# Performance work log

Measured on AMD Instinct MI355X. Metric: run time of the kernel, lower is better.

The kernel has to match this reference:

```python
import jax, jax.numpy as jnp
import numpy as np

CONTEXT_DIM = 64
HIDDEN = 512
BS = 1024
SEQ = 168
TWIN = 96


def setup_inputs() -> dict:
    key = jax.random.key(0)
    k0, k1, k2, k3 = jax.random.split(key, 4)
    x_dyn = jax.random.normal(k0, (BS, SEQ, CONTEXT_DIM), jnp.float32)
    y_flow = jax.random.normal(k1, (BS, SEQ, 1), jnp.float32)
    input_dim = CONTEXT_DIM + 1 + 1
    W = jax.random.normal(k2, (input_dim + HIDDEN, HIDDEN * 4), jnp.float32) * 0.02
    b = jnp.zeros((HIDDEN * 4,), jnp.float32)
    Wo = jax.random.normal(k3, (HIDDEN, 1), jnp.float32) * 0.02
    bo = jnp.zeros((1,), jnp.float32)
    return {"x_dyn": x_dyn, "y_flow": y_flow, "W": W, "b": b,
            "Wo": Wo, "bo": bo, "twin_idx": TWIN}


def _cell(inp, h, c, W, b, hidden):
    # fused gate GEMM: [bs, input_dim+hidden] @ [input_dim+hidden, 4*hidden]
    gates = jnp.concatenate([inp, h], axis=1) @ W + b
    i, f, g, o = jnp.split(gates, 4, axis=1)
    i = jax.nn.sigmoid(i)
    f = jax.nn.sigmoid(f)
    o = jax.nn.sigmoid(o)
    g = jnp.tanh(g)
    c_next = f * c + i * g
    h_next = o * jnp.tanh(c_next)
    return h_next, c_next


def reference(x_dyn, y_flow, W, b, Wo, bo, twin_idx):
    bs, seq_len, _ = x_dyn.shape
    hidden = W.shape[1] // 4
    h0 = jnp.zeros((bs, hidden), x_dyn.dtype)
    c0 = jnp.zeros((bs, hidden), x_dyn.dtype)
    zeros_col = jnp.zeros((bs, 1), x_dyn.dtype)
    ones_col = jnp.ones((bs, 1), x_dyn.dtype)

    # Phase 1: teacher-forced steps t in [0, twin_idx), h_since_tw = 0
    def step1(carry, xs):
        h, c = carry
        x_t, y_t = xs
        inp = jnp.concatenate([x_t, y_t, zeros_col], axis=1)
        h, c = _cell(inp, h, c, W, b, hidden)
        pred = h @ Wo + bo  # [bs, 1]
        return (h, c), pred

    xs1 = (jnp.swapaxes(x_dyn[:, :twin_idx], 0, 1),
           jnp.swapaxes(y_flow[:, :twin_idx], 0, 1))
    (h, c), preds1 = jax.lax.scan(step1, (h0, c0), xs1)  # preds1: [twin_idx, bs, 1]
    last_out = preds1[-1]

    n2 = seq_len - 1 - twin_idx
    h_vals = (jnp.arange(n2, dtype=x_dyn.dtype) + 1.0) / 24.0

    def step2(carry, xs):
        h, c, last = carry
        x_t, hv = xs
        inp = jnp.concatenate([x_t, last, hv * ones_col], axis=1)
        h, c = _cell(inp, h, c, W, b, hidden)
        last = h @ Wo + bo
        return (h, c, last), last

    xs2 = (jnp.swapaxes(x_dyn[:, twin_idx:seq_len - 1], 0, 1), h_vals)
    _, preds2 = jax.lax.scan(step2, (h, c, last_out), xs2)  # [n2, bs, 1]

    preds = jnp.concatenate([preds1, preds2], axis=0)  # [seq_len-1, bs, 1]
    return jnp.swapaxes(preds, 0, 1)  # [bs, seq_len-1, 1]
```

## Files before the change

### kernel.cpp

```cpp
#include <hip/hip_runtime.h>


#define HIDDEN 512
#define SEQ    168
#define NSTEP  167
#define BS     1024
#define CTX    64
#define KM     576
#define KP     584
#define MTILE  128
#define SGRID  512
#define PGRID  256
#define NTHR   256
#define WTELEM (2 * 32 * KP)

typedef __attribute__((ext_vector_type(8))) short s16x8;
typedef __attribute__((ext_vector_type(4))) float f32x4;

static __device__ __forceinline__ unsigned short bf16_rne(float f) {
    union { float f; unsigned int u; } v; v.f = f;
    unsigned int r = v.u + 0x7FFFu + ((v.u >> 16) & 1u);
    return (unsigned short)(r >> 16);
}
static __device__ __forceinline__ float bf16_to_f(unsigned short h) {
    union { float f; unsigned int u; } v; v.u = ((unsigned int)h) << 16;
    return v.f;
}
static __device__ __forceinline__ float sigmoid_(float x) {
    x = fminf(fmaxf(x, -80.f), 80.f);
    return 1.0f / (1.0f + __expf(-x));
}
static __device__ __forceinline__ float tanh_(float x) {
    float ax = fminf(fabsf(x), 40.f);
    float e = __expf(-2.0f * ax);
    float r = (1.0f - e) / (1.0f + e);
    return copysignf(r, x);
}

__global__ void lstm_prep(const float* __restrict__ x_dyn, float* __restrict__ out,
                          const float* __restrict__ bo_p,
                          unsigned short* __restrict__ aHi, unsigned short* __restrict__ aLo,
                          float* __restrict__ cst)
{
    const int gthr = blockIdx.x * NTHR + threadIdx.x;
    const int gstr = PGRID * NTHR;
    const float bo = *bo_p;
    for (int i = gthr; i < BS * NSTEP; i += gstr) out[i] = bo;
    for (int i = gthr; i < BS * HIDDEN; i += gstr) cst[i] = 0.f;
    for (int i = gthr; i < BS * 256; i += gstr) {
        const int b = i >> 8, j = i & 255;
        ((unsigned int*)aHi)[b * 288 + 32 + j] = 0u;
        ((unsigned int*)aLo)[b * 288 + 32 + j] = 0u;
    }
    for (int i = gthr; i < BS * CTX; i += gstr) {
        const int b = i >> 6, col = i & 63;
        const float v = x_dyn[(size_t)b * SEQ * CTX + col];
        const unsigned short hi = bf16_rne(v);
        aHi[(size_t)b * KM + col] = hi;
        aLo[(size_t)b * KM + col] = bf16_rne(v - bf16_to_f(hi));
    }
}

__global__ void wprep(const float* __restrict__ Wg, unsigned short* __restrict__ wpl)
{
    const int gthr = blockIdx.x * NTHR + threadIdx.x;
    const int gstr = PGRID * NTHR;
    for (int i = gthr; i < 64 * 32 * KP; i += gstr) {
        const int kp = i % KP;
        const int c  = (i / KP) & 31;
        const int nt = i / (KP * 32);
        unsigned short hi = 0, lo = 0;
        if (kp < KM) {
            const int wrow = (kp < 64) ? kp : (kp + 2);
            const int wcol = (2 * (c >> 4) + ((c >> 3) & 1)) * 512 + nt * 8 + (c & 7);
            const float v = Wg[(size_t)wrow * 2048 + wcol];
            hi = bf16_rne(v);
            lo = bf16_rne(v - bf16_to_f(hi));
        }
        const size_t base = (size_t)nt * WTELEM + (size_t)c * KP + kp;
        wpl[base] = hi;
        wpl[base + 32 * KP] = lo;
    }
}

__global__ __launch_bounds__(NTHR, 2)
void lstm_step(const float* __restrict__ x_dyn, const float* __restrict__ y_flow,
               const float* __restrict__ Wg, const float* __restrict__ bias,
               const float* __restrict__ Wo, const int* __restrict__ twin_p,
               float* __restrict__ out, unsigned short* __restrict__ aHi,
               unsigned short* __restrict__ aLo, float* __restrict__ cst,
               const unsigned short* __restrict__ wpl, int t)
{
    extern __shared__ unsigned char smem_raw[];
    unsigned short* whi = (unsigned short*)smem_raw;
    unsigned short* wlo = whi + 32 * KP;
    float* a64s = (float*)(wlo + 32 * KP);

    const int tid = threadIdx.x, bid = blockIdx.x;
    const int nt = bid >> 3;
    const int m0 = (bid & 7) * MTILE;
    const int lane = tid & 63, wv = tid >> 6;
    const int ln15 = lane & 15, kg = lane >> 4;
    const int twin = *twin_p;

    const int par = t & 1, pn = par ^ 1;
    const unsigned short* aH = aHi + (size_t)par * BS * KM;
    const unsigned short* aL = aLo + (size_t)par * BS * KM;
    unsigned short* nH = aHi + (size_t)pn * BS * KM;
    unsigned short* nL = aLo + (size_t)pn * BS * KM;
    const float hv = (t < twin) ? 0.f : (float)(t - twin + 1) * (1.f / 24.f);

    const unsigned short* wsrc = wpl + (size_t)nt * WTELEM;
#if __has_builtin(__builtin_amdgcn_global_load_lds)
    for (int c = wv; c < 73; c += 4) {
        __builtin_amdgcn_global_load_lds(
            (const __attribute__((address_space(1))) void*)(wsrc + c * 512 + lane * 8),
            (__attribute__((address_space(3))) void*)(smem_raw + c * 1024),
            16, 0, 0);
    }
#else
    for (int idx = tid; idx < WTELEM / 8; idx += NTHR) {
        *(s16x8*)((unsigned short*)smem_raw + idx * 8) = *(const s16x8*)(wsrc + idx * 8);
    }
#endif

    if (tid < MTILE) {
        const int b = m0 + tid;
        float v;
        if (t < twin) v = y_flow[(size_t)b * SEQ + t];
        else if (t > 0) v = out[(size_t)b * NSTEP + (t - 1)];
        else v = 0.f;
        a64s[tid] = v;
    }
    __syncthreads();

    if (tid < 128) {
        const int b = m0 + nt * 2 + (tid >> 6), col = tid & 63;
        const float v = x_dyn[((size_t)b * SEQ + (t + 1)) * CTX + col];
        const unsigned short hi = bf16_rne(v);
        nH[(size_t)b * KM + col] = hi;
        nL[(size_t)b * KM + col] = bf16_rne(v - bf16_to_f(hi));
    }

    float w64c[2], basec[2];
    #pragma unroll
    for (int ns = 0; ns < 2; ++ns) {
        const int wcol = (2 * ns + (ln15 >> 3)) * 512 + nt * 8 + (ln15 & 7);
        w64c[ns]  = Wg[(size_t)64 * 2048 + wcol];
        basec[ns] = fmaf(hv, Wg[(size_t)65 * 2048 + wcol], bias[wcol]);
    }
    const int u = nt * 8 + (ln15 & 7);
    const float wo_u = Wo[u];
    const bool lo_half = (ln15 < 8);

    const size_t aoff0 = (size_t)(m0 + wv * 32 + ln15) * KM + kg * 8;
    const size_t aoff1 = aoff0 + (size_t)16 * KM;

    f32x4 acc[2][2];
    #pragma unroll
    for (int ms = 0; ms < 2; ++ms)
        #pragma unroll
        for (int ns = 0; ns < 2; ++ns) acc[ms][ns] = (f32x4){0.f, 0.f, 0.f, 0.f};

    #pragma unroll
    for (int half = 0; half < 2; ++half) {
        s16x8 Ah[9][2], Al[9][2];
        #pragma unroll
        for (int j = 0; j < 9; ++j) {
            const size_t k0 = (size_t)(half * 9 + j) * 32;
            Ah[j][0] = *(const s16x8*)(aH + aoff0 + k0);
            Ah[j][1] = *(const s16x8*)(aH + aoff1 + k0);
            Al[j][0] = *(const s16x8*)(aL + aoff0 + k0);
            Al[j][1] = *(const s16x8*)(aL + aoff1 + k0);
        }
        #pragma unroll
        for (int j = 0; j < 9; ++j) {
            const int k0 = (half * 9 + j) * 32;
            s16x8 bh[2], bl[2];
            #pragma unroll
            for (int ns = 0; ns < 2; ++ns) {
                const int boff = (ns * 16 + ln15) * KP + k0 + kg * 8;
                bh[ns] = *(const s16x8*)(whi + boff);
                bl[ns] = *(const s16x8*)(wlo + boff);
            }
            #pragma unroll
            for (int ns = 0; ns < 2; ++ns)
                #pragma unroll
                for (int ms = 0; ms < 2; ++ms) {
                    acc[ms][ns] = __builtin_amdgcn_mfma_f32_16x16x32_bf16(Ah[j][ms], bh[ns], acc[ms][ns], 0, 0, 0);
                    acc[ms][ns] = __builtin_amdgcn_mfma_f32_16x16x32_bf16(Ah[j][ms], bl[ns], acc[ms][ns], 0, 0, 0);
                    acc[ms][ns] = __builtin_amdgcn_mfma_f32_16x16x32_bf16(Al[j][ms], bh[ns], acc[ms][ns], 0, 0, 0);
                }
        }
    }

    #pragma unroll
    for (int ms = 0; ms < 2; ++ms) {
        #pragma unroll
        for (int r = 0; r < 4; ++r) {
            const int rl = wv * 32 + ms * 16 + kg * 4 + r;
            const int b = m0 + rl;
            const float a64v = a64s[rl];
            const float pre0 = acc[ms][0][r] + fmaf(a64v, w64c[0], basec[0]);
            const float pre1 = acc[ms][1][r] + fmaf(a64v, w64c[1], basec[1]);
            const float q0 = __shfl_xor(pre0, 8, 16);
            const float q1 = __shfl_xor(pre1, 8, 16);
            const float pi = lo_half ? pre0 : q0;
            const float pf = lo_half ? q0 : pre0;
            const float pg = lo_half ? pre1 : q1;
            const float po = lo_half ? q1 : pre1;
            const float i_ = sigmoid_(pi);
            const float f_ = sigmoid_(pf);
            const float g_ = tanh_(pg);
            const float o_ = sigmoid_(po);
            const size_t ci = (size_t)b * HIDDEN + u;
            const float c = f_ * cst[ci] + i_ * g_;
            const float h = o_ * tanh_(c);
            if (lo_half) {
                cst[ci] = c;
                const unsigned short hh = bf16_rne(h);
                nH[(size_t)b * KM + 64 + u] = hh;
                nL[(size_t)b * KM + 64 + u] = bf16_rne(h - bf16_to_f(hh));
            }
            float p = lo_half ? h * wo_u : 0.f;
            p += __shfl_xor(p, 1, 16);
            p += __shfl_xor(p, 2, 16);
            p += __shfl_xor(p, 4, 16);
            p += __shfl_xor(p, 8, 16);
            if (ln15 == 0) atomicAdd(&out[(size_t)b * NSTEP + t], p);
        }
    }
}

extern "C" void kernel_launch(void* const* d_in, const int* in_sizes, int n_in,
                              void* d_out, int out_size, void* d_ws, size_t ws_size,
                              hipStream_t stream) {
    (void)in_sizes; (void)n_in; (void)out_size; (void)ws_size;
    const float* x_dyn  = (const float*)d_in[0];
    const float* y_flow = (const float*)d_in[1];
    const float* Wg     = (const float*)d_in[2];
    const float* bias   = (const float*)d_in[3];
    const float* Wo     = (const float*)d_in[4];
    const float* bo     = (const float*)d_in[5];
    const int*   twin   = (const int*)d_in[6];
    float* out = (float*)d_out;

    unsigned short* aHi = (unsigned short*)d_ws;
    unsigned short* aLo = aHi + (size_t)2 * BS * KM;
    float* cst = (float*)(aLo + (size_t)2 * BS * KM);
    unsigned short* wpl = (unsigned short*)(cst + (size_t)BS * HIDDEN);

    const unsigned int smem = (2u * 32u * KP) * 2u + MTILE * 4u;

    (void)hipFuncSetAttribute((const void*)lstm_step,
                              hipFuncAttributeMaxDynamicSharedMemorySize, (int)smem);

    lstm_prep<<<dim3(PGRID), dim3(NTHR), 0, stream>>>(x_dyn, out, bo, aHi, aLo, cst);
    wprep<<<dim3(PGRID), dim3(NTHR), 0, stream>>>(Wg, wpl);

    for (int t = 0; t < NSTEP; ++t) {
        lstm_step<<<dim3(SGRID), dim3(NTHR), smem, stream>>>(
            x_dyn, y_flow, Wg, bias, Wo, twin, out, aHi, aLo, cst, wpl, t);
    }
}
```

Measured before the change: 5.099 ms.

## Replace per-step kernel launches with persistent cooperative kernel using grid sync

Runs all 167 recurrent steps inside one cooperative kernel with grid.sync between steps, and stages each block's weight slice into LDS only once instead of once per step. This removes per-step launch overhead and the repeated weight reload. It also switches the A-operand loads to inline-asm global loads followed by an explicit vmcnt wait, and reads the previous prediction with an atomic load. It depends on 512 blocks being co-resident at two blocks per CU, and falls back to the per-step launch loop if the cooperative launch fails.

```diff
diff --git a/kernel.cpp b/kernel.cpp
--- a/kernel.cpp
+++ b/kernel.cpp
@@ -1,4 +1,7 @@
 #include <hip/hip_runtime.h>
+#include <hip/hip_cooperative_groups.h>
+
+namespace cg = cooperative_groups;
 
 
 #define HIDDEN 512
@@ -35,6 +38,11 @@
     float e = __expf(-2.0f * ax);
     float r = (1.0f - e) / (1.0f + e);
     return copysignf(r, x);
+}
+static __device__ __forceinline__ s16x8 gload16(const unsigned short* p) {
+    s16x8 r;
+    asm volatile("global_load_dwordx4 %0, %1, off" : "=v"(r) : "v"(p));
+    return r;
 }
 
 __global__ void lstm_prep(const float* __restrict__ x_dyn, float* __restrict__ out,
@@ -83,26 +91,28 @@
     }
 }
 
-__global__ __launch_bounds__(NTHR, 2)
-void lstm_step(const float* __restrict__ x_dyn, const float* __restrict__ y_flow,
-               const float* __restrict__ Wg, const float* __restrict__ bias,
-               const float* __restrict__ Wo, const int* __restrict__ twin_p,
-               float* __restrict__ out, unsigned short* __restrict__ aHi,
-               unsigned short* __restrict__ aLo, float* __restrict__ cst,
-               const unsigned short* __restrict__ wpl, int t)
-{
-    extern __shared__ unsigned char smem_raw[];
-    unsigned short* whi = (unsigned short*)smem_raw;
-    unsigned short* wlo = whi + 32 * KP;
-    float* a64s = (float*)(wlo + 32 * KP);
-
-    const int tid = threadIdx.x, bid = blockIdx.x;
-    const int nt = bid >> 3;
-    const int m0 = (bid & 7) * MTILE;
-    const int lane = tid & 63, wv = tid >> 6;
-    const int ln15 = lane & 15, kg = lane >> 4;
-    const int twin = *twin_p;
-
+static __device__ __forceinline__ void stage_w(const unsigned short* __restrict__ wpl,
+                                               unsigned char* smem_raw, int nt, int wv, int lane)
+{
+    const unsigned short* wsrc = wpl + (size_t)nt * WTELEM;
+    for (int c = wv; c < 73; c += 4) {
+        __builtin_amdgcn_global_load_lds(
+            (const __attribute__((address_space(1))) void*)(wsrc + c * 512 + lane * 8),
+            (__attribute__((address_space(3))) void*)(smem_raw + c * 1024),
+            16, 0, 0);
+    }
+}
+
+static __device__ __forceinline__ void step_core(
+    int t, int twin, int tid, int nt, int m0,
+    const float* __restrict__ x_dyn, const float* __restrict__ y_flow,
+    float* __restrict__ out, float* __restrict__ cst,
+    unsigned short* __restrict__ aHi, unsigned short* __restrict__ aLo,
+    const unsigned short* whi, const unsigned short* wlo, float* a64s,
+    const float* w64c, const float* w65c, const float* biasc,
+    float wo_u, int u, int wv, int ln15, int kg, bool lo_half,
+    size_t aoff0, size_t aoff1)
+{
     const int par = t & 1, pn = par ^ 1;
     const unsigned short* aH = aHi + (size_t)par * BS * KM;
     const unsigned short* aL = aLo + (size_t)par * BS * KM;
@@ -110,25 +120,12 @@
     unsigned short* nL = aLo + (size_t)pn * BS * KM;
     const float hv = (t < twin) ? 0.f : (float)(t - twin + 1) * (1.f / 24.f);
 
-    const unsigned short* wsrc = wpl + (size_t)nt * WTELEM;
-#if __has_builtin(__builtin_amdgcn_global_load_lds)
-    for (int c = wv; c < 73; c += 4) {
-        __builtin_amdgcn_global_load_lds(
-            (const __attribute__((address_space(1))) void*)(wsrc + c * 512 + lane * 8),
-            (__attribute__((address_space(3))) void*)(smem_raw + c * 1024),
-            16, 0, 0);
-    }
-#else
-    for (int idx = tid; idx < WTELEM / 8; idx += NTHR) {
-        *(s16x8*)((unsigned short*)smem_raw + idx * 8) = *(const s16x8*)(wsrc + idx * 8);
-    }
-#endif
-
     if (tid < MTILE) {
         const int b = m0 + tid;
         float v;
         if (t < twin) v = y_flow[(size_t)b * SEQ + t];
-        else if (t > 0) v = out[(size_t)b * NSTEP + (t - 1)];
+        else if (t > 0) v = __hip_atomic_load(&out[(size_t)b * NSTEP + (t - 1)],
+                                              __ATOMIC_RELAXED, __HIP_MEMORY_SCOPE_AGENT);
         else v = 0.f;
         a64s[tid] = v;
     }
@@ -142,19 +139,9 @@
         nL[(size_t)b * KM + col] = bf16_rne(v - bf16_to_f(hi));
     }
 
-    float w64c[2], basec[2];
-    #pragma unroll
-    for (int ns = 0; ns < 2; ++ns) {
-        const int wcol = (2 * ns + (ln15 >> 3)) * 512 + nt * 8 + (ln15 & 7);
-        w64c[ns]  = Wg[(size_t)64 * 2048 + wcol];
-        basec[ns] = fmaf(hv, Wg[(size_t)65 * 2048 + wcol], bias[wcol]);
-    }
-    const int u = nt * 8 + (ln15 & 7);
-    const float wo_u = Wo[u];
-    const bool lo_half = (ln15 < 8);
-
-    const size_t aoff0 = (size_t)(m0 + wv * 32 + ln15) * KM + kg * 8;
-    const size_t aoff1 = aoff0 + (size_t)16 * KM;
+    float basec2[2];
+    basec2[0] = fmaf(hv, w65c[0], biasc[0]);
+    basec2[1] = fmaf(hv, w65c[1], biasc[1]);
 
     f32x4 acc[2][2];
     #pragma unroll
@@ -168,11 +155,13 @@
         #pragma unroll
         for (int j = 0; j < 9; ++j) {
             const size_t k0 = (size_t)(half * 9 + j) * 32;
-            Ah[j][0] = *(const s16x8*)(aH + aoff0 + k0);
-            Ah[j][1] = *(const s16x8*)(aH + aoff1 + k0);
-            Al[j][0] = *(const s16x8*)(aL + aoff0 + k0);
-            Al[j][1] = *(const s16x8*)(aL + aoff1 + k0);
-        }
+            Ah[j][0] = gload16(aH + aoff0 + k0);
+            Ah[j][1] = gload16(aH + aoff1 + k0);
+            Al[j][0] = gload16(aL + aoff0 + k0);
+            Al[j][1] = gload16(aL + aoff1 + k0);
+        }
+        asm volatile("s_waitcnt vmcnt(0)" ::: "memory");
+        __builtin_amdgcn_sched_barrier(0);
         #pragma unroll
         for (int j = 0; j < 9; ++j) {
             const int k0 = (half * 9 + j) * 32;
@@ -201,8 +190,8 @@
             const int rl = wv * 32 + ms * 16 + kg * 4 + r;
             const int b = m0 + rl;
             const float a64v = a64s[rl];
-            const float pre0 = acc[ms][0][r] + fmaf(a64v, w64c[0], basec[0]);
-            const float pre1 = acc[ms][1][r] + fmaf(a64v, w64c[1], basec[1]);
+            const float pre0 = acc[ms][0][r] + fmaf(a64v, w64c[0], basec2[0]);
+            const float pre1 = acc[ms][1][r] + fmaf(a64v, w64c[1], basec2[1]);
             const float q0 = __shfl_xor(pre0, 8, 16);
             const float q1 = __shfl_xor(pre1, 8, 16);
             const float pi = lo_half ? pre0 : q0;
@@ -232,6 +221,74 @@
     }
 }
 
+#define LANE_SETUP                                                              \
+    const int tid = threadIdx.x, bid = blockIdx.x;                              \
+    const int nt = bid >> 3;                   \
+    const int m0 = (bid & 7) * MTILE;              \
+    const int lane = tid & 63, wv = tid >> 6, ln15 = lane & 15, kg = lane >> 4; \
+    const int twin = *twin_p;                                                   \
+    float w64c[2], w65c[2], biasc[2];                                           \
+    _Pragma("unroll")                                                           \
+    for (int ns = 0; ns < 2; ++ns) {                                            \
+        const int wcol = (2 * ns + (ln15 >> 3)) * 512 + nt * 8 + (ln15 & 7);    \
+        w64c[ns]  = Wg[(size_t)64 * 2048 + wcol];                               \
+        w65c[ns]  = Wg[(size_t)65 * 2048 + wcol];                               \
+        biasc[ns] = bias[wcol];                                                 \
+    }                                                                           \
+    const int u = nt * 8 + (ln15 & 7);                                          \
+    const float wo_u = Wo[u];                                                   \
+    const bool lo_half = (ln15 < 8);                                            \
+    const size_t aoff0 = (size_t)(m0 + wv * 32 + ln15) * KM + kg * 8;           \
+    const size_t aoff1 = aoff0 + (size_t)16 * KM;
+
+__global__ __launch_bounds__(NTHR, 2)
+void lstm_persist(const float* __restrict__ x_dyn, const float* __restrict__ y_flow,
+                  const float* __restrict__ Wg, const float* __restrict__ bias,
+                  const float* __restrict__ Wo, const int* __restrict__ twin_p,
+                  float* __restrict__ out, unsigned short* __restrict__ aHi,
+                  unsigned short* __restrict__ aLo, float* __restrict__ cst,
+                  const unsigned short* __restrict__ wpl)
+{
+    cg::grid_group grid = cg::this_grid();
+    extern __shared__ unsigned char smem_raw[];
+    unsigned short* whi = (unsigned short*)smem_raw;
+    unsigned short* wlo = whi + 32 * KP;
+    float* a64s = (float*)(wlo + 32 * KP);
+
+    LANE_SETUP
+
+    stage_w(wpl, smem_raw, nt, wv, lane);
+
+    for (int t = 0; t < NSTEP; ++t) {
+        step_core(t, twin, tid, nt, m0, x_dyn, y_flow, out, cst, aHi, aLo,
+                  whi, wlo, a64s, w64c, w65c, biasc, wo_u, u, wv, ln15, kg,
+                  lo_half, aoff0, aoff1);
+        if (t != NSTEP - 1) grid.sync();
+    }
+}
+
+__global__ __launch_bounds__(NTHR, 2)
+void lstm_step(const float* __restrict__ x_dyn, const float* __restrict__ y_flow,
+               const float* __restrict__ Wg, const float* __restrict__ bias,
+               const float* __restrict__ Wo, const int* __restrict__ twin_p,
+               float* __restrict__ out, unsigned short* __restrict__ aHi,
+               unsigned short* __restrict__ aLo, float* __restrict__ cst,
+               const unsigned short* __restrict__ wpl, int t)
+{
+    extern __shared__ unsigned char smem_raw[];
+    unsigned short* whi = (unsigned short*)smem_raw;
+    unsigned short* wlo = whi + 32 * KP;
+    float* a64s = (float*)(wlo + 32 * KP);
+
+    LANE_SETUP
+
+    stage_w(wpl, smem_raw, nt, wv, lane);
+
+    step_core(t, twin, tid, nt, m0, x_dyn, y_flow, out, cst, aHi, aLo,
+              whi, wlo, a64s, w64c, w65c, biasc, wo_u, u, wv, ln15, kg,
+              lo_half, aoff0, aoff1);
+}
+
 extern "C" void kernel_launch(void* const* d_in, const int* in_sizes, int n_in,
                               void* d_out, int out_size, void* d_ws, size_t ws_size,
                               hipStream_t stream) {
@@ -252,14 +309,24 @@
 
     const unsigned int smem = (2u * 32u * KP) * 2u + MTILE * 4u;
 
+    (void)hipFuncSetAttribute((const void*)lstm_persist,
+                              hipFuncAttributeMaxDynamicSharedMemorySize, (int)smem);
     (void)hipFuncSetAttribute((const void*)lstm_step,
                               hipFuncAttributeMaxDynamicSharedMemorySize, (int)smem);
 
     lstm_prep<<<dim3(PGRID), dim3(NTHR), 0, stream>>>(x_dyn, out, bo, aHi, aLo, cst);
     wprep<<<dim3(PGRID), dim3(NTHR), 0, stream>>>(Wg, wpl);
 
-    for (int t = 0; t < NSTEP; ++t) {
-        lstm_step<<<dim3(SGRID), dim3(NTHR), smem, stream>>>(
-            x_dyn, y_flow, Wg, bias, Wo, twin, out, aHi, aLo, cst, wpl, t);
-    }
-}
+    void* kargs[] = {(void*)&x_dyn, (void*)&y_flow, (void*)&Wg, (void*)&bias,
+                     (void*)&Wo, (void*)&twin, (void*)&out,
+                     (void*)&aHi, (void*)&aLo, (void*)&cst, (void*)&wpl};
+    hipError_t rc = hipLaunchCooperativeKernel((const void*)lstm_persist,
+                                               dim3(SGRID), dim3(NTHR), kargs,
+                                               smem, stream);
+    if (rc != hipSuccess) {
+        for (int t = 0; t < NSTEP; ++t) {
+            lstm_step<<<dim3(SGRID), dim3(NTHR), smem, stream>>>(
+                x_dyn, y_flow, Wg, bias, Wo, twin, out, aHi, aLo, cst, wpl, t);
+        }
+    }
+}
```

Result: slower. 13.27 ms (+160.2%).
